# Kernel tuning notes

Measured on AMD Instinct MI355X. Metric: run time of the kernel, lower is better.

## Reference

```python
import jax, jax.numpy as jnp
import numpy as np

B, N, C = 4, 4096, 2048
EPS = 1e-5  # torch.nn.LayerNorm default


def setup_inputs() -> dict:
    key = jax.random.key(0)
    kx, = jax.random.split(key, 1)
    x = jax.random.normal(kx, (B, N, C), dtype=jnp.float32)
    gamma = jnp.ones((C,), dtype=jnp.float32)   # LayerNorm weight
    beta = jnp.zeros((C,), dtype=jnp.float32)   # LayerNorm bias
    return {"x": x, "gamma": gamma, "beta": beta}


def reference(x, gamma, beta):
    # The original repeats x to (B,N,N,C), applies a (no-op on the diagonal)
    # triu mask, FFTs every row over C, and extracts the (n,n) diagonal.
    # The diagonal rows are exactly the unmasked originals, so this equals:
    #   LayerNorm(real(fft(x, axis=-1)))
    y = jnp.fft.fft(x, axis=-1).real  # (B,N,C)
    mu = jnp.mean(y, axis=-1, keepdims=True)
    var = jnp.mean(jnp.square(y - mu), axis=-1, keepdims=True)  # biased, as torch LN
    return (y - mu) * jax.lax.rsqrt(var + EPS) * gamma + beta
```

## Files before the change

kernel.cpp:

```cpp
#include <hip/hip_runtime.h>
#include <math.h>


#define TPB 256
#define CD  2048

__device__ __forceinline__ float2 cadd(float2 a, float2 b){ return make_float2(a.x+b.x, a.y+b.y); }
__device__ __forceinline__ float2 csub(float2 a, float2 b){ return make_float2(a.x-b.x, a.y-b.y); }

__device__ __forceinline__ void dft8(const float2* z, float2* y)
{
    const float C8 = 0.70710678118654752440f;
    float2 a0=cadd(z[0],z[4]), a1=cadd(z[1],z[5]), a2=cadd(z[2],z[6]), a3=cadd(z[3],z[7]);
    float2 b0=csub(z[0],z[4]), b1=csub(z[1],z[5]), b2=csub(z[2],z[6]), b3=csub(z[3],z[7]);
    float2 t1=make_float2(C8*(b1.x+b1.y), C8*(b1.y-b1.x));
    float2 t2=make_float2(b2.y, -b2.x);
    float2 t3=make_float2(C8*(b3.y-b3.x), -C8*(b3.x+b3.y));
    {
        float pr=a0.x+a2.x, pi=a0.y+a2.y, mr=a0.x-a2.x, mi=a0.y-a2.y;
        float qr=a1.x+a3.x, qi=a1.y+a3.y, nr=a1.x-a3.x, ni=a1.y-a3.y;
        y[0]=make_float2(pr+qr,pi+qi); y[2]=make_float2(mr+ni,mi-nr);
        y[4]=make_float2(pr-qr,pi-qi); y[6]=make_float2(mr-ni,mi+nr);
    }
    {
        float pr=b0.x+t2.x, pi=b0.y+t2.y, mr=b0.x-t2.x, mi=b0.y-t2.y;
        float qr=t1.x+t3.x, qi=t1.y+t3.y, nr=t1.x-t3.x, ni=t1.y-t3.y;
        y[1]=make_float2(pr+qr,pi+qi); y[3]=make_float2(mr+ni,mi-nr);
        y[5]=make_float2(pr-qr,pi-qi); y[7]=make_float2(mr-ni,mi+nr);
    }
}

__device__ __forceinline__ void make_tw(float th1, float* cw, float* sw)
{
    float s1, c1;
    __sincosf(th1, &s1, &c1);
    cw[0]=1.f;                       sw[0]=0.f;
    cw[1]=c1;                        sw[1]=s1;
    cw[2]=c1*c1-s1*s1;               sw[2]=2.f*c1*s1;
    cw[4]=cw[2]*cw[2]-sw[2]*sw[2];   sw[4]=2.f*cw[2]*sw[2];
    cw[3]=c1*cw[2]-s1*sw[2];         sw[3]=s1*cw[2]+c1*sw[2];
    cw[5]=c1*cw[4]-s1*sw[4];         sw[5]=s1*cw[4]+c1*sw[4];
    cw[6]=cw[2]*cw[4]-sw[2]*sw[4];   sw[6]=sw[2]*cw[4]+cw[2]*sw[4];
    cw[7]=cw[3]*cw[4]-sw[3]*sw[4];   sw[7]=sw[3]*cw[4]+cw[3]*sw[4];
}

template<int OFFM>
__device__ __forceinline__ void r8_store(float2* Lw, const float2* y,
                                         const float* cw, const float* sw)
{
    Lw[0] = y[0];
#pragma unroll
    for (int r = 1; r < 8; ++r)
        Lw[OFFM*r] = make_float2(cw[r]*y[r].x - sw[r]*y[r].y,
                                 cw[r]*y[r].y + sw[r]*y[r].x);
}

__global__ __launch_bounds__(TPB, 8) void fourier_ln_kernel(
    const float* __restrict__ x,
    const float* __restrict__ gamma,
    const float* __restrict__ beta,
    float* __restrict__ out)
{
    __shared__ float2 L[2304];
    __shared__ float rmem[16];

    const int t  = threadIdx.x;
    const int t8 = t >> 3;
    const long long row0 = 2LL * (long long)blockIdx.x;
    const float* __restrict__ x0 = x + row0 * CD;
    const float* __restrict__ x1 = x0 + CD;

    float2 z[8], y[8];
#pragma unroll
    for (int r = 0; r < 8; ++r) {
        const int k = t + 256*r;
        z[r] = make_float2(x0[k], x1[k]);
    }

    float2* const Lr = L + (t + t8);
    float cw[8], sw[8];

    make_tw(-3.06796157577128245943e-3f * (float)t, cw, sw);
    dft8(z, y);
    r8_store<1>(L + 9*t, y, cw, sw);
    __syncthreads();
#pragma unroll
    for (int r = 0; r < 8; ++r) z[r] = Lr[288*r];
    __syncthreads();

    make_tw(-2.45436926061702596755e-2f * (float)t8, cw, sw);
    dft8(z, y);
    r8_store<9>(L + ((t & 7) + 72*t8), y, cw, sw);
    __syncthreads();
#pragma unroll
    for (int r = 0; r < 8; ++r) z[r] = Lr[288*r];
    __syncthreads();

    dft8(z, y);
    {
        const int q = t & 63, p = t >> 6;
        make_tw(-1.96349540849362077404e-1f * (float)p, cw, sw);
        r8_store<72>(L + (q + (q >> 3) + 576*p), y, cw, sw);
    }
    __syncthreads();

    const int u   = t >> 1;
    const int sig = (t & 1) ? ((u == 0) ? 128 : 256 - u) : u;

    float2* const Lsig = L + (sig + (sig >> 3));
#pragma unroll
    for (int r = 0; r < 8; ++r) z[r] = Lsig[288*r];

    float2 Z[8];
    {
        float pr=z[0].x+z[4].x, pi=z[0].y+z[4].y, mr=z[0].x-z[4].x, mi=z[0].y-z[4].y;
        float qr=z[2].x+z[6].x, qi=z[2].y+z[6].y, nr=z[2].x-z[6].x, ni=z[2].y-z[6].y;
        Z[0]=make_float2(pr+qr,pi+qi); Z[2]=make_float2(mr+ni,mi-nr);
        Z[4]=make_float2(pr-qr,pi-qi); Z[6]=make_float2(mr-ni,mi+nr);
    }
    {
        float pr=z[1].x+z[5].x, pi=z[1].y+z[5].y, mr=z[1].x-z[5].x, mi=z[1].y-z[5].y;
        float qr=z[3].x+z[7].x, qi=z[3].y+z[7].y, nr=z[3].x-z[7].x, ni=z[3].y-z[7].y;
        Z[1]=make_float2(pr+qr,pi+qi); Z[3]=make_float2(mr+ni,mi-nr);
        Z[5]=make_float2(pr-qr,pi-qi); Z[7]=make_float2(mr-ni,mi+nr);
    }

    float s0=0.f, ss0=0.f, s1=0.f, ss1=0.f;
#pragma unroll
    for (int j = 0; j < 8; ++j) {
        float vx = __shfl_xor(Z[7-j].x, 1, 64);
        float vy = __shfl_xor(Z[7-j].y, 1, 64);
        const int ja = (8-j) & 7;
        float ax = (t == 0) ? Z[ja].x : Z[7-j].x;
        float ay = (t == 0) ? Z[ja].y : Z[7-j].y;
        vx = (t < 2) ? ax : vx;
        vy = (t < 2) ? ay : vy;
        float a = 0.5f*(Z[j].x + vx);
        float b = 0.5f*(Z[j].y + vy);
        Lsig[288*j] = make_float2(a, b);
        s0+=a; ss0+=a*a; s1+=b; ss1+=b*b;
    }

#pragma unroll
    for (int off = 32; off > 0; off >>= 1) {
        s0  += __shfl_down(s0,  off, 64);
        ss0 += __shfl_down(ss0, off, 64);
        s1  += __shfl_down(s1,  off, 64);
        ss1 += __shfl_down(ss1, off, 64);
    }
    const int wave = t >> 6;
    if ((t & 63) == 0) {
        rmem[4*wave+0]=s0; rmem[4*wave+1]=ss0; rmem[4*wave+2]=s1; rmem[4*wave+3]=ss1;
    }
    __syncthreads();

    const float4 g0 = ((const float4*)gamma)[t];
    const float4 b0 = ((const float4*)beta )[t];
    const float4 g1 = ((const float4*)gamma)[t + 256];
    const float4 b1 = ((const float4*)beta )[t + 256];

    float S0=0.f, SS0=0.f, S1=0.f, SS1=0.f;
#pragma unroll
    for (int w = 0; w < 4; ++w) {
        S0+=rmem[4*w+0]; SS0+=rmem[4*w+1]; S1+=rmem[4*w+2]; SS1+=rmem[4*w+3];
    }
    const float inv = 1.0f/(float)CD;
    const float mu0 = S0*inv, mu1 = S1*inv;
    const float r0 = rsqrtf(SS0*inv - mu0*mu0 + 1e-5f);
    const float r1 = rsqrtf(SS1*inv - mu1*mu1 + 1e-5f);

    const float2* const Ls = L + (4*t + (t >> 1));
    float4* __restrict__ o0 = (float4*)(out + row0*CD);
    float4* __restrict__ o1 = (float4*)(out + (row0+1)*CD);
#pragma unroll
    for (int h = 0; h < 2; ++h) {
        float2 p0 = Ls[1152*h + 0];
        float2 p1 = Ls[1152*h + 1];
        float2 p2 = Ls[1152*h + 2];
        float2 p3 = Ls[1152*h + 3];
        const float4 g = h ? g1 : g0;
        const float4 be = h ? b1 : b0;
        float4 v0, v1;
        v0.x=(p0.x-mu0)*r0*g.x+be.x; v1.x=(p0.y-mu1)*r1*g.x+be.x;
        v0.y=(p1.x-mu0)*r0*g.y+be.y; v1.y=(p1.y-mu1)*r1*g.y+be.y;
        v0.z=(p2.x-mu0)*r0*g.z+be.z; v1.z=(p2.y-mu1)*r1*g.z+be.z;
        v0.w=(p3.x-mu0)*r0*g.w+be.w; v1.w=(p3.y-mu1)*r1*g.w+be.w;
        o0[t + 256*h] = v0;
        o1[t + 256*h] = v1;
    }
}

extern "C" void kernel_launch(void* const* d_in, const int* in_sizes, int n_in,
                              void* d_out, int out_size, void* d_ws, size_t ws_size,
                              hipStream_t stream) {
    (void)in_sizes; (void)n_in; (void)d_ws; (void)ws_size; (void)out_size;
    const float* x     = (const float*)d_in[0];
    const float* gamma = (const float*)d_in[1];
    const float* beta  = (const float*)d_in[2];
    float* out = (float*)d_out;

    const int total_rows = 4 * 4096;
    const int blocks = total_rows / 2;
    fourier_ln_kernel<<<blocks, TPB, 0, stream>>>(x, gamma, beta, out);
}
```

Baseline: 231.5 us.

## Decompose FFT into per-wave 512-point sub-FFTs with wave-local sync

Restructures the 2048-point FFT as a decimation where each wavefront computes an independent 512-point FFT over a strided subset (n = 4e+256r+w) in its own LDS region. The block-wide __syncthreads between the first radix-8 stages are replaced by an s_waitcnt lgkmcnt(0). A final radix-4 combine with computed twiddles merges the four sub-FFTs. This aims to cut block barrier stalls, at the cost of strided global loads and reliance on LDS ordering within a wave. The wave-local fence may be insufficient for cross-lane LDS visibility on some compilers.

```diff
diff --git a/kernel.cpp b/kernel.cpp
--- a/kernel.cpp
+++ b/kernel.cpp
@@ -4,6 +4,8 @@
 
 #define TPB 256
 #define CD  2048
+
+#define WAVE_SYNC() asm volatile("s_waitcnt lgkmcnt(0)" ::: "memory")
 
 __device__ __forceinline__ float2 cadd(float2 a, float2 b){ return make_float2(a.x+b.x, a.y+b.y); }
 __device__ __forceinline__ float2 csub(float2 a, float2 b){ return make_float2(a.x-b.x, a.y-b.y); }
@@ -65,7 +67,9 @@
     __shared__ float rmem[16];
 
     const int t  = threadIdx.x;
-    const int t8 = t >> 3;
+    const int e  = t & 63;
+    const int w  = t >> 6;
+    const int e8 = e >> 3;
     const long long row0 = 2LL * (long long)blockIdx.x;
     const float* __restrict__ x0 = x + row0 * CD;
     const float* __restrict__ x1 = x0 + CD;
@@ -73,59 +77,83 @@
     float2 z[8], y[8];
 #pragma unroll
     for (int r = 0; r < 8; ++r) {
-        const int k = t + 256*r;
-        z[r] = make_float2(x0[k], x1[k]);
-    }
-
-    float2* const Lr = L + (t + t8);
+        const int n = 4*e + 256*r + w;
+        z[r] = make_float2(x0[n], x1[n]);
+    }
+
     float cw[8], sw[8];
-
-    make_tw(-3.06796157577128245943e-3f * (float)t, cw, sw);
+    float2* const Lw = L + 576*w;
+
+    make_tw(-1.22718463030851329843e-2f * (float)e, cw, sw);
     dft8(z, y);
-    r8_store<1>(L + 9*t, y, cw, sw);
-    __syncthreads();
-#pragma unroll
-    for (int r = 0; r < 8; ++r) z[r] = Lr[288*r];
-    __syncthreads();
-
-    make_tw(-2.45436926061702596755e-2f * (float)t8, cw, sw);
+    r8_store<1>(Lw + 9*e, y, cw, sw);
+    WAVE_SYNC();
+
+    {
+        const float2* Lr = Lw + e + e8;
+#pragma unroll
+        for (int k = 0; k < 8; ++k) z[k] = Lr[72*k];
+    }
+    make_tw(-9.81747704246810387019e-2f * (float)e8, cw, sw);
     dft8(z, y);
-    r8_store<9>(L + ((t & 7) + 72*t8), y, cw, sw);
-    __syncthreads();
-#pragma unroll
-    for (int r = 0; r < 8; ++r) z[r] = Lr[288*r];
-    __syncthreads();
-
-    dft8(z, y);
-    {
-        const int q = t & 63, p = t >> 6;
-        make_tw(-1.96349540849362077404e-1f * (float)p, cw, sw);
-        r8_store<72>(L + (q + (q >> 3) + 576*p), y, cw, sw);
+    r8_store<9>(Lw + (e & 7) + 72*e8, y, cw, sw);
+    WAVE_SYNC();
+
+    {
+        float2* Lr = Lw + e + e8;
+#pragma unroll
+        for (int k = 0; k < 8; ++k) z[k] = Lr[72*k];
+        dft8(z, y);
+#pragma unroll
+        for (int r = 0; r < 8; ++r) Lr[72*r] = y[r];
     }
     __syncthreads();
 
     const int u   = t >> 1;
     const int sig = (t & 1) ? ((u == 0) ? 128 : 256 - u) : u;
-
-    float2* const Lsig = L + (sig + (sig >> 3));
-#pragma unroll
-    for (int r = 0; r < 8; ++r) z[r] = Lsig[288*r];
+    const int po  = sig + (sig >> 3);
+
+    float2 XA[4], XB[4];
+#pragma unroll
+    for (int l = 0; l < 4; ++l) {
+        XA[l] = L[576*l + po];
+        XB[l] = L[576*l + po + 288];
+    }
+
+    float c1, s1;
+    __sincosf(-3.06796157577128245943e-3f * (float)sig, &s1, &c1);
+    const float c2 = c1*c1 - s1*s1, s2 = 2.f*c1*s1;
+    const float c3 = c1*c2 - s1*s2, s3 = s1*c2 + c1*s2;
+    const float C8 = 0.70710678118654752440f;
 
     float2 Z[8];
     {
-        float pr=z[0].x+z[4].x, pi=z[0].y+z[4].y, mr=z[0].x-z[4].x, mi=z[0].y-z[4].y;
-        float qr=z[2].x+z[6].x, qi=z[2].y+z[6].y, nr=z[2].x-z[6].x, ni=z[2].y-z[6].y;
-        Z[0]=make_float2(pr+qr,pi+qi); Z[2]=make_float2(mr+ni,mi-nr);
-        Z[4]=make_float2(pr-qr,pi-qi); Z[6]=make_float2(mr-ni,mi+nr);
-    }
-    {
-        float pr=z[1].x+z[5].x, pi=z[1].y+z[5].y, mr=z[1].x-z[5].x, mi=z[1].y-z[5].y;
-        float qr=z[3].x+z[7].x, qi=z[3].y+z[7].y, nr=z[3].x-z[7].x, ni=z[3].y-z[7].y;
-        Z[1]=make_float2(pr+qr,pi+qi); Z[3]=make_float2(mr+ni,mi-nr);
-        Z[5]=make_float2(pr-qr,pi-qi); Z[7]=make_float2(mr-ni,mi+nr);
-    }
-
-    float s0=0.f, ss0=0.f, s1=0.f, ss1=0.f;
+        float2 T0 = XA[0];
+        float2 T1 = make_float2(c1*XA[1].x - s1*XA[1].y, c1*XA[1].y + s1*XA[1].x);
+        float2 T2 = make_float2(c2*XA[2].x - s2*XA[2].y, c2*XA[2].y + s2*XA[2].x);
+        float2 T3 = make_float2(c3*XA[3].x - s3*XA[3].y, c3*XA[3].y + s3*XA[3].x);
+        float2 a = cadd(T0,T2), b = csub(T0,T2), cc = cadd(T1,T3), d = csub(T1,T3);
+        Z[0] = cadd(a,cc);
+        Z[2] = make_float2(b.x + d.y, b.y - d.x);
+        Z[4] = csub(a,cc);
+        Z[6] = make_float2(b.x - d.y, b.y + d.x);
+    }
+    {
+        const float u1x = C8*(c1+s1), u1y = C8*(s1-c1);
+        const float u3x = C8*(s3-c3), u3y = -C8*(s3+c3);
+        float2 T0 = XB[0];
+        float2 T1 = make_float2(u1x*XB[1].x - u1y*XB[1].y, u1x*XB[1].y + u1y*XB[1].x);
+        float2 T2 = make_float2(s2*XB[2].x + c2*XB[2].y, s2*XB[2].y - c2*XB[2].x);
+        float2 T3 = make_float2(u3x*XB[3].x - u3y*XB[3].y, u3x*XB[3].y + u3y*XB[3].x);
+        float2 a = cadd(T0,T2), b = csub(T0,T2), cc = cadd(T1,T3), d = csub(T1,T3);
+        Z[1] = cadd(a,cc);
+        Z[3] = make_float2(b.x + d.y, b.y - d.x);
+        Z[5] = csub(a,cc);
+        Z[7] = make_float2(b.x - d.y, b.y + d.x);
+    }
+
+    float2* const Lsig = L + po;
+    float s0=0.f, ss0=0.f, sum1=0.f, ss1=0.f;
 #pragma unroll
     for (int j = 0; j < 8; ++j) {
         float vx = __shfl_xor(Z[7-j].x, 1, 64);
@@ -138,19 +166,18 @@
         float a = 0.5f*(Z[j].x + vx);
         float b = 0.5f*(Z[j].y + vy);
         Lsig[288*j] = make_float2(a, b);
-        s0+=a; ss0+=a*a; s1+=b; ss1+=b*b;
+        s0+=a; ss0+=a*a; sum1+=b; ss1+=b*b;
     }
 
 #pragma unroll
     for (int off = 32; off > 0; off >>= 1) {
-        s0  += __shfl_down(s0,  off, 64);
-        ss0 += __shfl_down(ss0, off, 64);
-        s1  += __shfl_down(s1,  off, 64);
-        ss1 += __shfl_down(ss1, off, 64);
-    }
-    const int wave = t >> 6;
+        s0   += __shfl_down(s0,   off, 64);
+        ss0  += __shfl_down(ss0,  off, 64);
+        sum1 += __shfl_down(sum1, off, 64);
+        ss1  += __shfl_down(ss1,  off, 64);
+    }
     if ((t & 63) == 0) {
-        rmem[4*wave+0]=s0; rmem[4*wave+1]=ss0; rmem[4*wave+2]=s1; rmem[4*wave+3]=ss1;
+        rmem[4*w+0]=s0; rmem[4*w+1]=ss0; rmem[4*w+2]=sum1; rmem[4*w+3]=ss1;
     }
     __syncthreads();
 
@@ -161,8 +188,8 @@
 
     float S0=0.f, SS0=0.f, S1=0.f, SS1=0.f;
 #pragma unroll
-    for (int w = 0; w < 4; ++w) {
-        S0+=rmem[4*w+0]; SS0+=rmem[4*w+1]; S1+=rmem[4*w+2]; SS1+=rmem[4*w+3];
+    for (int v = 0; v < 4; ++v) {
+        S0+=rmem[4*v+0]; SS0+=rmem[4*v+1]; S1+=rmem[4*v+2]; SS1+=rmem[4*v+3];
     }
     const float inv = 1.0f/(float)CD;
     const float mu0 = S0*inv, mu1 = S1*inv;
@@ -178,7 +205,7 @@
         float2 p1 = Ls[1152*h + 1];
         float2 p2 = Ls[1152*h + 2];
         float2 p3 = Ls[1152*h + 3];
-        const float4 g = h ? g1 : g0;
+        const float4 g  = h ? g1 : g0;
         const float4 be = h ? b1 : b0;
         float4 v0, v1;
         v0.x=(p0.x-mu0)*r0*g.x+be.x; v1.x=(p0.y-mu1)*r1*g.x+be.x;
```

Result: no change. 233.7 us (+0.9%).
